# Kernel optimization log

Measured on AMD Instinct MI355X. Metric: run time of the kernel, lower is better.

Reference implementation:

```python
import jax, jax.numpy as jnp
import numpy as np

B, L, C, H = 2, 512, 256, 8
D = C // H
LN_EPS = 1e-5


def setup_inputs() -> dict:
    key = jax.random.key(0)
    ks = jax.random.split(key, 9)
    s = lambda fan: 1.0 / np.sqrt(fan)
    return {
        "x": jax.random.normal(ks[0], (B, L, C), dtype=jnp.float32),
        "relative_pos": jax.random.normal(ks[1], (B, L, L, C), dtype=jnp.float32),
        "w_qkv": jax.random.normal(ks[2], (3 * C, C), dtype=jnp.float32) * s(C),
        "w_rel": jax.random.normal(ks[3], (H, C), dtype=jnp.float32) * s(C),
        "b_rel": jax.random.normal(ks[4], (H,), dtype=jnp.float32) * 0.02,
        "ln_gamma": jnp.ones((H,), dtype=jnp.float32),
        "ln_beta": jnp.zeros((H,), dtype=jnp.float32),
        "w_proj": jax.random.normal(ks[5], (C, C), dtype=jnp.float32) * s(C),
        "b_proj": jnp.zeros((C,), dtype=jnp.float32),
    }


def reference(x, relative_pos, w_qkv, w_rel, b_rel, ln_gamma, ln_beta, w_proj, b_proj):
    scale = D ** -0.5
    # qkv projection: [B,L,3C] -> [3,B,H,L,D]
    qkv = (x @ w_qkv.T).reshape(B, L, 3, H, D).transpose(2, 0, 3, 1, 4)
    q, k, v = qkv[0], qkv[1], qkv[2]
    # relative bias: Linear -> exact GELU -> LayerNorm over head dim
    rel = relative_pos @ w_rel.T + b_rel          # [B,L,L,H]
    rel = jax.nn.gelu(rel, approximate=False)
    mu = jnp.mean(rel, axis=-1, keepdims=True)
    var = jnp.mean(jnp.square(rel - mu), axis=-1, keepdims=True)
    rel = (rel - mu) * jax.lax.rsqrt(var + LN_EPS) * ln_gamma + ln_beta
    rel = rel.transpose(0, 3, 1, 2)               # [B,H,L,L]
    # attention (bias added pre-scale, matching the original)
    attn = (jnp.einsum("bhld,bhmd->bhlm", q, k) + rel) * scale
    attn = jax.nn.softmax(attn, axis=-1)
    out = jnp.einsum("bhlm,bhmd->bhld", attn, v)  # [B,H,L,D]
    out = out.transpose(0, 2, 1, 3).reshape(B, L, C)
    return out @ w_proj.T + b_proj
```

## Files before the change

### kernel.cpp

```cpp
#include <hip/hip_runtime.h>
#include <hip/hip_bf16.h>
#include <math.h>

#define BB 2
#define LL 512
#define CC 256
#define HH 8
#define DD 32
#define LN_EPS 1e-5f
#define SCALE 0.17677669529663687f
#define RSQRT2 0.70710678118654752f

__global__ __launch_bounds__(256) void k1_qkv(const float* __restrict__ x,
                                              const float* __restrict__ w,
                                              float* __restrict__ qkv_out) {
    __shared__ float xs[16][64];
    __shared__ float wsd[16][64];
    const int row0 = blockIdx.x * 64;
    const int col0 = blockIdx.y * 64;
    const int t  = threadIdx.x;
    const int ry = t >> 4;
    const int cx = t & 15;
    const int lr = t >> 2;
    const int lq = t & 3;
    float acc[4][4] = {};
    for (int k0 = 0; k0 < 256; k0 += 16) {
        float4 xv = *(const float4*)(x + (row0 + lr) * 256 + k0 + 4 * lq);
        float4 wv = *(const float4*)(w + (col0 + lr) * 256 + k0 + 4 * lq);
        xs[4*lq+0][lr] = xv.x; xs[4*lq+1][lr] = xv.y;
        xs[4*lq+2][lr] = xv.z; xs[4*lq+3][lr] = xv.w;
        wsd[4*lq+0][lr] = wv.x; wsd[4*lq+1][lr] = wv.y;
        wsd[4*lq+2][lr] = wv.z; wsd[4*lq+3][lr] = wv.w;
        __syncthreads();
#pragma unroll
        for (int kk = 0; kk < 16; ++kk) {
            float4 a  = *(const float4*)&xs[kk][4*ry];
            float4 bb = *(const float4*)&wsd[kk][4*cx];
            float av[4] = {a.x, a.y, a.z, a.w};
            float bv[4] = {bb.x, bb.y, bb.z, bb.w};
#pragma unroll
            for (int rr = 0; rr < 4; ++rr)
#pragma unroll
                for (int cc = 0; cc < 4; ++cc)
                    acc[rr][cc] = fmaf(av[rr], bv[cc], acc[rr][cc]);
        }
        __syncthreads();
    }
#pragma unroll
    for (int rr = 0; rr < 4; ++rr) {
        const int row = row0 + 4*ry + rr;
        const int b = row >> 9, l = row & 511;
#pragma unroll
        for (int cc = 0; cc < 4; ++cc) {
            const int o = col0 + 4*cx + cc;
            const int three = o >> 8;
            const int hh = (o >> 5) & 7;
            const int dd = o & 31;
            int idx;
            if (three == 1)
                idx = 262144 + ((b*8 + hh)*32 + dd)*512 + l;
            else
                idx = three * 262144 + ((b*8 + hh)*512 + l)*32 + dd;
            qkv_out[idx] = acc[rr][cc];
        }
    }
}

__global__ __launch_bounds__(256) void k2_rel(const float* __restrict__ rp,
                                              const float* __restrict__ wr,
                                              const float* __restrict__ br,
                                              const float* __restrict__ gam_p,
                                              const float* __restrict__ bet_p,
                                              float* __restrict__ rel_t) {
    __shared__ float st[8][65];
    const int t    = threadIdx.x;
    const int lane = t & 63;
    const int wid  = t >> 6;
    const int blk  = blockIdx.x;
    const int jt = blk & 7;
    const int i  = (blk >> 3) & 511;
    const int b  = blk >> 12;
    const int j0 = jt << 6;
    const int chunk = lane & 31;
    const int jh    = lane >> 5;
    const int h     = lane & 7;

    float wreg[8][8];
    {
        const float4* wr4 = (const float4*)wr;
#pragma unroll
        for (int hh = 0; hh < 8; ++hh) {
            float4 w0 = wr4[hh*64 + chunk*2];
            float4 w1 = wr4[hh*64 + chunk*2 + 1];
            wreg[hh][0]=w0.x; wreg[hh][1]=w0.y; wreg[hh][2]=w0.z; wreg[hh][3]=w0.w;
            wreg[hh][4]=w1.x; wreg[hh][5]=w1.y; wreg[hh][6]=w1.z; wreg[hh][7]=w1.w;
        }
    }
    const float brv = br[h], gmv = gam_p[h], btv = bet_p[h];

    const float* base = rp + ((long)(b*512 + i)*512 + (j0 + wid*16 + jh)) * 256
                           + chunk*8;
    float4 a0 = *(const float4*)(base);
    float4 a1 = *(const float4*)(base + 4);
#pragma unroll
    for (int it = 0; it < 8; ++it) {
        float4 n0 = a0, n1 = a1;
        if (it < 7) {
            const float* np = base + (2*(it+1))*256;
            n0 = *(const float4*)(np);
            n1 = *(const float4*)(np + 4);
        }
        float acc[8];
#pragma unroll
        for (int hh = 0; hh < 8; ++hh) {
            float s = 0.f;
            s = fmaf(a0.x, wreg[hh][0], s);
            s = fmaf(a0.y, wreg[hh][1], s);
            s = fmaf(a0.z, wreg[hh][2], s);
            s = fmaf(a0.w, wreg[hh][3], s);
            s = fmaf(a1.x, wreg[hh][4], s);
            s = fmaf(a1.y, wreg[hh][5], s);
            s = fmaf(a1.z, wreg[hh][6], s);
            s = fmaf(a1.w, wreg[hh][7], s);
            acc[hh] = s;
        }
#pragma unroll
        for (int hh = 0; hh < 8; ++hh) acc[hh] += __shfl_xor(acc[hh], 1);
#pragma unroll
        for (int hh = 0; hh < 8; ++hh) acc[hh] += __shfl_xor(acc[hh], 2);
#pragma unroll
        for (int hh = 0; hh < 8; ++hh) acc[hh] += __shfl_xor(acc[hh], 4);
        float v0 = (h & 1) ? acc[1] : acc[0];
        float v1 = (h & 1) ? acc[3] : acc[2];
        float v2 = (h & 1) ? acc[5] : acc[4];
        float v3 = (h & 1) ? acc[7] : acc[6];
        float u0 = (h & 2) ? v1 : v0;
        float u1 = (h & 2) ? v3 : v2;
        float tot = (h & 4) ? u1 : u0;
        tot += __shfl_xor(tot, 8);
        tot += __shfl_xor(tot, 16);

        const float r = tot + brv;
        const float g = 0.5f * r * (1.0f + erff(r * RSQRT2));
        float sg = g, sg2 = g * g;
        sg += __shfl_xor(sg, 1); sg2 += __shfl_xor(sg2, 1);
        sg += __shfl_xor(sg, 2); sg2 += __shfl_xor(sg2, 2);
        sg += __shfl_xor(sg, 4); sg2 += __shfl_xor(sg2, 4);
        const float mu  = sg * 0.125f;
        const float var = fmaf(sg2, 0.125f, -mu * mu);
        const float o = fmaf((g - mu) * rsqrtf(var + LN_EPS), gmv, btv);
        if ((lane & 31) < 8)
            st[h][wid*16 + 2*it + jh] = o;
        a0 = n0; a1 = n1;
    }
    __syncthreads();
    const int h2 = t >> 5, j2 = t & 31;
    const long orow = ((long)(b*8 + h2) * 512 + i) * 512 + j0;
    rel_t[orow + j2]      = st[h2][j2];
    rel_t[orow + j2 + 32] = st[h2][j2 + 32];
}

__global__ __launch_bounds__(256) void k3_attn(const float* __restrict__ qg,
                                               const float* __restrict__ kt,
                                               const float* __restrict__ vg,
                                               const float* __restrict__ rel_t,
                                               float* __restrict__ outg) {
    __shared__ float p_lds[4][512];
    const int lane = threadIdx.x & 63;
    const int wid  = threadIdx.x >> 6;
    const int row  = blockIdx.x * 4 + wid;
    const int b = row >> 12;
    const int h = (row >> 9) & 7;
    const int i = row & 511;
    const int bh = b*8 + h;

    const float* qp = qg + (bh*512 + i) * 32;
    float qs[32];
#pragma unroll
    for (int dd = 0; dd < 8; ++dd) {
        float4 q4 = *(const float4*)(qp + 4*dd);
        qs[4*dd+0]=q4.x; qs[4*dd+1]=q4.y; qs[4*dd+2]=q4.z; qs[4*dd+3]=q4.w;
    }
    const float4* kt4  = (const float4*)(kt + (long)bh * 32 * 512);
    const float4* rel4 = (const float4*)(rel_t + ((long)bh * 512 + i) * 512);

    float4 s0 = {0.f,0.f,0.f,0.f}, s1 = {0.f,0.f,0.f,0.f};
#pragma unroll
    for (int dd = 0; dd < 32; ++dd) {
        float4 ka = kt4[dd*128 + lane];
        float4 kb = kt4[dd*128 + 64 + lane];
        const float qd = qs[dd];
        s0.x = fmaf(qd, ka.x, s0.x); s0.y = fmaf(qd, ka.y, s0.y);
        s0.z = fmaf(qd, ka.z, s0.z); s0.w = fmaf(qd, ka.w, s0.w);
        s1.x = fmaf(qd, kb.x, s1.x); s1.y = fmaf(qd, kb.y, s1.y);
        s1.z = fmaf(qd, kb.z, s1.z); s1.w = fmaf(qd, kb.w, s1.w);
    }
    float4 r0 = rel4[lane], r1 = rel4[64 + lane];
    s0.x = (s0.x + r0.x) * SCALE; s0.y = (s0.y + r0.y) * SCALE;
    s0.z = (s0.z + r0.z) * SCALE; s0.w = (s0.w + r0.w) * SCALE;
    s1.x = (s1.x + r1.x) * SCALE; s1.y = (s1.y + r1.y) * SCALE;
    s1.z = (s1.z + r1.z) * SCALE; s1.w = (s1.w + r1.w) * SCALE;
    float m = fmaxf(fmaxf(fmaxf(s0.x, s0.y), fmaxf(s0.z, s0.w)),
                    fmaxf(fmaxf(s1.x, s1.y), fmaxf(s1.z, s1.w)));
    m = fmaxf(m, __shfl_xor(m, 1));
    m = fmaxf(m, __shfl_xor(m, 2));
    m = fmaxf(m, __shfl_xor(m, 4));
    m = fmaxf(m, __shfl_xor(m, 8));
    m = fmaxf(m, __shfl_xor(m, 16));
    m = fmaxf(m, __shfl_xor(m, 32));
    s0.x = __expf(s0.x - m); s0.y = __expf(s0.y - m);
    s0.z = __expf(s0.z - m); s0.w = __expf(s0.w - m);
    s1.x = __expf(s1.x - m); s1.y = __expf(s1.y - m);
    s1.z = __expf(s1.z - m); s1.w = __expf(s1.w - m);
    float sum = ((s0.x + s0.y) + (s0.z + s0.w)) + ((s1.x + s1.y) + (s1.z + s1.w));
    sum += __shfl_xor(sum, 1);
    sum += __shfl_xor(sum, 2);
    sum += __shfl_xor(sum, 4);
    sum += __shfl_xor(sum, 8);
    sum += __shfl_xor(sum, 16);
    sum += __shfl_xor(sum, 32);
    const float inv = 1.0f / sum;
    s0.x *= inv; s0.y *= inv; s0.z *= inv; s0.w *= inv;
    s1.x *= inv; s1.y *= inv; s1.z *= inv; s1.w *= inv;
    *(float4*)&p_lds[wid][4*lane]       = s0;
    *(float4*)&p_lds[wid][256 + 4*lane] = s1;
    __syncthreads();

    const int d = lane & 31;
    const int half = lane >> 5;
    const float* vp = vg + (long)(bh*512) * 32 + (half * 256) * 32 + d;
    const float* pw = &p_lds[wid][half * 256];
    float a0 = 0.f, a1 = 0.f, a2 = 0.f, a3 = 0.f;
#pragma unroll 4
    for (int jj = 0; jj < 256; jj += 4) {
        a0 = fmaf(pw[jj + 0], vp[(jj + 0) * 32], a0);
        a1 = fmaf(pw[jj + 1], vp[(jj + 1) * 32], a1);
        a2 = fmaf(pw[jj + 2], vp[(jj + 2) * 32], a2);
        a3 = fmaf(pw[jj + 3], vp[(jj + 3) * 32], a3);
    }
    float acc = (a0 + a1) + (a2 + a3);
    acc += __shfl_xor(acc, 32);
    if (lane < 32)
        outg[(b*512 + i) * 256 + h * 32 + d] = acc;
}

__global__ __launch_bounds__(256) void k4_proj(const float* __restrict__ a_in,
                                               const float* __restrict__ w,
                                               const float* __restrict__ bp,
                                               float* __restrict__ outg) {
    __shared__ float xs[16][64];
    __shared__ float wsd[16][64];
    const int row0 = blockIdx.x * 64;
    const int col0 = blockIdx.y * 64;
    const int t  = threadIdx.x;
    const int ry = t >> 4;
    const int cx = t & 15;
    const int lr = t >> 2;
    const int lq = t & 3;
    float acc[4][4] = {};
    for (int k0 = 0; k0 < 256; k0 += 16) {
        float4 xv = *(const float4*)(a_in + (row0 + lr) * 256 + k0 + 4 * lq);
        float4 wv = *(const float4*)(w + (col0 + lr) * 256 + k0 + 4 * lq);
        xs[4*lq+0][lr] = xv.x; xs[4*lq+1][lr] = xv.y;
        xs[4*lq+2][lr] = xv.z; xs[4*lq+3][lr] = xv.w;
        wsd[4*lq+0][lr] = wv.x; wsd[4*lq+1][lr] = wv.y;
        wsd[4*lq+2][lr] = wv.z; wsd[4*lq+3][lr] = wv.w;
        __syncthreads();
#pragma unroll
        for (int kk = 0; kk < 16; ++kk) {
            float4 a  = *(const float4*)&xs[kk][4*ry];
            float4 bb = *(const float4*)&wsd[kk][4*cx];
            float av[4] = {a.x, a.y, a.z, a.w};
            float bv[4] = {bb.x, bb.y, bb.z, bb.w};
#pragma unroll
            for (int rr = 0; rr < 4; ++rr)
#pragma unroll
                for (int cc = 0; cc < 4; ++cc)
                    acc[rr][cc] = fmaf(av[rr], bv[cc], acc[rr][cc]);
        }
        __syncthreads();
    }
#pragma unroll
    for (int rr = 0; rr < 4; ++rr) {
        const int row = row0 + 4*ry + rr;
#pragma unroll
        for (int cc = 0; cc < 4; ++cc) {
            const int col = col0 + 4*cx + cc;
            outg[row * 256 + col] = acc[rr][cc] + bp[col];
        }
    }
}

extern "C" void kernel_launch(void* const* d_in, const int* in_sizes, int n_in,
                              void* d_out, int out_size, void* d_ws, size_t ws_size,
                              hipStream_t stream) {
    const float* x      = (const float*)d_in[0];
    const float* rp     = (const float*)d_in[1];
    const float* w_qkv  = (const float*)d_in[2];
    const float* w_rel  = (const float*)d_in[3];
    const float* b_rel  = (const float*)d_in[4];
    const float* gamma  = (const float*)d_in[5];
    const float* beta   = (const float*)d_in[6];
    const float* w_proj = (const float*)d_in[7];
    const float* b_proj = (const float*)d_in[8];
    float* out = (float*)d_out;
    float* ws  = (float*)d_ws;

    float* q     = ws;
    float* kk    = ws + 262144;
    float* vv    = ws + 524288;
    float* rel_t = ws + 786432;
    float* attn  = ws + 786432 + 4194304;

    k1_qkv<<<dim3(16, 12), 256, 0, stream>>>(x, w_qkv, q);
    k2_rel<<<8192, 256, 0, stream>>>(rp, w_rel, b_rel, gamma, beta, rel_t);
    k3_attn<<<2048, 256, 0, stream>>>(q, kk, vv, rel_t, attn);
    k4_proj<<<dim3(16, 4), 256, 0, stream>>>(attn, w_proj, b_proj, out);
}
```

Baseline: 766.0 us.

## Fuse relative-bias computation into attention kernel, keeping bias rows in LDS

Merges the relative-position bias kernel and the attention kernel into one. Each 512-thread block handles one (b,i) query row: eight waves first compute the GELU+LayerNorm bias for all 512 keys and all 8 heads into shared memory, then each wave runs attention for one head reading the bias from LDS. This removes the 16 MB global write and re-read of the intermediate bias tensor and one launch. The shuffle reduction is also reorganised to select values before the xor-2 and xor-4 stages, cutting shuffle count. In exchange there are fewer, larger blocks with a long serial 32-iteration loop per wave and heavier register use, which may lower occupancy on the bandwidth-bound relative_pos stream.

```diff
diff --git a/kernel.cpp b/kernel.cpp
--- a/kernel.cpp
+++ b/kernel.cpp
@@ -66,21 +66,21 @@
     }
 }
 
-__global__ __launch_bounds__(256) void k2_rel(const float* __restrict__ rp,
-                                              const float* __restrict__ wr,
-                                              const float* __restrict__ br,
-                                              const float* __restrict__ gam_p,
-                                              const float* __restrict__ bet_p,
-                                              float* __restrict__ rel_t) {
-    __shared__ float st[8][65];
+__global__ __launch_bounds__(512) void k23_fused(const float* __restrict__ rp,
+                                                 const float* __restrict__ wr,
+                                                 const float* __restrict__ br,
+                                                 const float* __restrict__ gam_p,
+                                                 const float* __restrict__ bet_p,
+                                                 const float* __restrict__ qg,
+                                                 const float* __restrict__ kt,
+                                                 const float* __restrict__ vg,
+                                                 float* __restrict__ outg) {
+    __shared__ float rel_lds[8 * 516];
     const int t    = threadIdx.x;
     const int lane = t & 63;
     const int wid  = t >> 6;
-    const int blk  = blockIdx.x;
-    const int jt = blk & 7;
-    const int i  = (blk >> 3) & 511;
-    const int b  = blk >> 12;
-    const int j0 = jt << 6;
+    const int b = blockIdx.x >> 9;
+    const int i = blockIdx.x & 511;
     const int chunk = lane & 31;
     const int jh    = lane >> 5;
     const int h     = lane & 7;
@@ -98,14 +98,14 @@
     }
     const float brv = br[h], gmv = gam_p[h], btv = bet_p[h];
 
-    const float* base = rp + ((long)(b*512 + i)*512 + (j0 + wid*16 + jh)) * 256
+    const float* base = rp + ((long)(b*512 + i)*512 + (wid*64 + jh)) * 256
                            + chunk*8;
     float4 a0 = *(const float4*)(base);
     float4 a1 = *(const float4*)(base + 4);
-#pragma unroll
-    for (int it = 0; it < 8; ++it) {
+#pragma unroll 2
+    for (int it = 0; it < 32; ++it) {
         float4 n0 = a0, n1 = a1;
-        if (it < 7) {
+        if (it < 31) {
             const float* np = base + (2*(it+1))*256;
             n0 = *(const float4*)(np);
             n1 = *(const float4*)(np + 4);
@@ -126,16 +126,15 @@
         }
 #pragma unroll
         for (int hh = 0; hh < 8; ++hh) acc[hh] += __shfl_xor(acc[hh], 1);
-#pragma unroll
-        for (int hh = 0; hh < 8; ++hh) acc[hh] += __shfl_xor(acc[hh], 2);
-#pragma unroll
-        for (int hh = 0; hh < 8; ++hh) acc[hh] += __shfl_xor(acc[hh], 4);
         float v0 = (h & 1) ? acc[1] : acc[0];
         float v1 = (h & 1) ? acc[3] : acc[2];
         float v2 = (h & 1) ? acc[5] : acc[4];
         float v3 = (h & 1) ? acc[7] : acc[6];
+        v0 += __shfl_xor(v0, 2); v1 += __shfl_xor(v1, 2);
+        v2 += __shfl_xor(v2, 2); v3 += __shfl_xor(v3, 2);
         float u0 = (h & 2) ? v1 : v0;
         float u1 = (h & 2) ? v3 : v2;
+        u0 += __shfl_xor(u0, 4); u1 += __shfl_xor(u1, 4);
         float tot = (h & 4) ? u1 : u0;
         tot += __shfl_xor(tot, 8);
         tot += __shfl_xor(tot, 16);
@@ -150,30 +149,12 @@
         const float var = fmaf(sg2, 0.125f, -mu * mu);
         const float o = fmaf((g - mu) * rsqrtf(var + LN_EPS), gmv, btv);
         if ((lane & 31) < 8)
-            st[h][wid*16 + 2*it + jh] = o;
+            rel_lds[h * 516 + wid*64 + 2*it + jh] = o;
         a0 = n0; a1 = n1;
     }
     __syncthreads();
-    const int h2 = t >> 5, j2 = t & 31;
-    const long orow = ((long)(b*8 + h2) * 512 + i) * 512 + j0;
-    rel_t[orow + j2]      = st[h2][j2];
-    rel_t[orow + j2 + 32] = st[h2][j2 + 32];
-}
-
-__global__ __launch_bounds__(256) void k3_attn(const float* __restrict__ qg,
-                                               const float* __restrict__ kt,
-                                               const float* __restrict__ vg,
-                                               const float* __restrict__ rel_t,
-                                               float* __restrict__ outg) {
-    __shared__ float p_lds[4][512];
-    const int lane = threadIdx.x & 63;
-    const int wid  = threadIdx.x >> 6;
-    const int row  = blockIdx.x * 4 + wid;
-    const int b = row >> 12;
-    const int h = (row >> 9) & 7;
-    const int i = row & 511;
-    const int bh = b*8 + h;
-
+
+    const int bh = b*8 + wid;
     const float* qp = qg + (bh*512 + i) * 32;
     float qs[32];
 #pragma unroll
@@ -181,8 +162,8 @@
         float4 q4 = *(const float4*)(qp + 4*dd);
         qs[4*dd+0]=q4.x; qs[4*dd+1]=q4.y; qs[4*dd+2]=q4.z; qs[4*dd+3]=q4.w;
     }
-    const float4* kt4  = (const float4*)(kt + (long)bh * 32 * 512);
-    const float4* rel4 = (const float4*)(rel_t + ((long)bh * 512 + i) * 512);
+    const float4* kt4 = (const float4*)(kt + (long)bh * 32 * 512);
+    float* relrow = &rel_lds[wid * 516];
 
     float4 s0 = {0.f,0.f,0.f,0.f}, s1 = {0.f,0.f,0.f,0.f};
 #pragma unroll
@@ -195,7 +176,8 @@
         s1.x = fmaf(qd, kb.x, s1.x); s1.y = fmaf(qd, kb.y, s1.y);
         s1.z = fmaf(qd, kb.z, s1.z); s1.w = fmaf(qd, kb.w, s1.w);
     }
-    float4 r0 = rel4[lane], r1 = rel4[64 + lane];
+    float4 r0 = *(const float4*)&relrow[4*lane];
+    float4 r1 = *(const float4*)&relrow[256 + 4*lane];
     s0.x = (s0.x + r0.x) * SCALE; s0.y = (s0.y + r0.y) * SCALE;
     s0.z = (s0.z + r0.z) * SCALE; s0.w = (s0.w + r0.w) * SCALE;
     s1.x = (s1.x + r1.x) * SCALE; s1.y = (s1.y + r1.y) * SCALE;
@@ -222,26 +204,25 @@
     const float inv = 1.0f / sum;
     s0.x *= inv; s0.y *= inv; s0.z *= inv; s0.w *= inv;
     s1.x *= inv; s1.y *= inv; s1.z *= inv; s1.w *= inv;
-    *(float4*)&p_lds[wid][4*lane]       = s0;
-    *(float4*)&p_lds[wid][256 + 4*lane] = s1;
-    __syncthreads();
+    *(float4*)&relrow[4*lane]       = s0;
+    *(float4*)&relrow[256 + 4*lane] = s1;
 
     const int d = lane & 31;
     const int half = lane >> 5;
-    const float* vp = vg + (long)(bh*512) * 32 + (half * 256) * 32 + d;
-    const float* pw = &p_lds[wid][half * 256];
-    float a0 = 0.f, a1 = 0.f, a2 = 0.f, a3 = 0.f;
+    const float* vp = vg + (long)bh * 512 * 32 + (half * 256) * 32 + d;
+    const float* pw = relrow + half * 256;
+    float a0s = 0.f, a1s = 0.f, a2s = 0.f, a3s = 0.f;
 #pragma unroll 4
     for (int jj = 0; jj < 256; jj += 4) {
-        a0 = fmaf(pw[jj + 0], vp[(jj + 0) * 32], a0);
-        a1 = fmaf(pw[jj + 1], vp[(jj + 1) * 32], a1);
-        a2 = fmaf(pw[jj + 2], vp[(jj + 2) * 32], a2);
-        a3 = fmaf(pw[jj + 3], vp[(jj + 3) * 32], a3);
-    }
-    float acc = (a0 + a1) + (a2 + a3);
+        a0s = fmaf(pw[jj + 0], vp[(jj + 0) * 32], a0s);
+        a1s = fmaf(pw[jj + 1], vp[(jj + 1) * 32], a1s);
+        a2s = fmaf(pw[jj + 2], vp[(jj + 2) * 32], a2s);
+        a3s = fmaf(pw[jj + 3], vp[(jj + 3) * 32], a3s);
+    }
+    float acc = (a0s + a1s) + (a2s + a3s);
     acc += __shfl_xor(acc, 32);
     if (lane < 32)
-        outg[(b*512 + i) * 256 + h * 32 + d] = acc;
+        outg[(b*512 + i) * 256 + wid * 32 + d] = acc;
 }
 
 __global__ __launch_bounds__(256) void k4_proj(const float* __restrict__ a_in,
@@ -306,14 +287,13 @@
     float* out = (float*)d_out;
     float* ws  = (float*)d_ws;
 
-    float* q     = ws;
-    float* kk    = ws + 262144;
-    float* vv    = ws + 524288;
-    float* rel_t = ws + 786432;
-    float* attn  = ws + 786432 + 4194304;
+    float* q    = ws;
+    float* kk   = ws + 262144;
+    float* vv   = ws + 524288;
+    float* attn = ws + 786432;
 
     k1_qkv<<<dim3(16, 12), 256, 0, stream>>>(x, w_qkv, q);
-    k2_rel<<<8192, 256, 0, stream>>>(rp, w_rel, b_rel, gamma, beta, rel_t);
-    k3_attn<<<2048, 256, 0, stream>>>(q, kk, vv, rel_t, attn);
+    k23_fused<<<1024, 512, 0, stream>>>(rp, w_rel, b_rel, gamma, beta,
+                                        q, kk, vv, attn);
     k4_proj<<<dim3(16, 4), 256, 0, stream>>>(attn, w_proj, b_proj, out);
 }
```

After: 762.3 us. Within noise of the previous version (-0.5%).
